# Optimization experiments

Hardware: AMD Instinct MI355X
Metric: run time of the kernel (lower is better)

The kernel has to match this reference:

```python
import jax, jax.numpy as jnp
import numpy as np

B, S, H, U = 32, 2048, 1024, 1024


def setup_inputs() -> dict:
    key = jax.random.key(0)
    ks = jax.random.split(key, 5)
    sc = 1.0 / np.sqrt(H)
    return {
        "hidden_t": jax.random.normal(ks[0], (B, H), jnp.float32),
        "hiddens": jax.random.normal(ks[1], (B, S, H), jnp.float32),
        "W1": jax.random.normal(ks[2], (H, U), jnp.float32) * sc,
        "b1": jnp.zeros((U,), jnp.float32),
        "W2": jax.random.normal(ks[3], (H, U), jnp.float32) * sc,
        "b2": jnp.zeros((U,), jnp.float32),
        "V": jax.random.normal(ks[4], (U, 1), jnp.float32) * sc,
        "bV": jnp.zeros((1,), jnp.float32),
    }


def reference(hidden_t, hiddens, W1, b1, W2, b2, V, bV):
    # proj of encoder states: [B,S,U]; proj of decoder state broadcast over time: [B,1,U]
    keys = jnp.einsum("bsh,hu->bsu", hiddens, W1) + b1
    query = (hidden_t @ W2 + b2)[:, None, :]
    score = jnp.tanh(keys + query) @ V + bV            # [B,S,1]
    attention_weights = jax.nn.softmax(score, axis=1)  # softmax over seq axis
    context_vector = jnp.sum(attention_weights * hiddens, axis=1)  # [B,H]
    return context_vector, attention_weights
```

## Files before the change

kernel.cpp:

```cpp
#include <hip/hip_runtime.h>
#include <hip/hip_bf16.h>
#include <cstdint>

#define S_LEN 2048
#define B_SZ  32
#define H_DIM 1024
#define U_DIM 1024

#define BM 128
#define BN 128
#define BK 64

using short8  = __attribute__((ext_vector_type(8))) short;
using floatx4 = __attribute__((ext_vector_type(4))) float;

typedef __attribute__((address_space(3))) void lds_void;
typedef const __attribute__((address_space(1))) void glb_void;
#define GLD16(g, s) __builtin_amdgcn_global_load_lds((glb_void*)(g), (lds_void*)(s), 16, 0, 0)

__device__ __forceinline__ unsigned short f32_to_bf16_rne(float f) {
    unsigned int u = __float_as_uint(f);
    unsigned int r = (u + 0x7fffu + ((u >> 16) & 1u)) >> 16;
    return (unsigned short)r;
}

__global__ __launch_bounds__(256)
void cast_hiddens_kernel(const float* __restrict__ src, unsigned short* __restrict__ dst) {
    const size_t i = ((size_t)blockIdx.x * 256 + threadIdx.x) * 8;
    float4 a = *(const float4*)(src + i);
    float4 b = *(const float4*)(src + i + 4);
    ushort4 lo, hi;
    lo.x = f32_to_bf16_rne(a.x); lo.y = f32_to_bf16_rne(a.y);
    lo.z = f32_to_bf16_rne(a.z); lo.w = f32_to_bf16_rne(a.w);
    hi.x = f32_to_bf16_rne(b.x); hi.y = f32_to_bf16_rne(b.y);
    hi.z = f32_to_bf16_rne(b.z); hi.w = f32_to_bf16_rne(b.w);
    *(ushort4*)(dst + i)     = lo;
    *(ushort4*)(dst + i + 4) = hi;
}

__global__ void transpose_cast_w1(const float* __restrict__ W1,
                                  unsigned short* __restrict__ W1t) {
    __shared__ float tile[32][33];
    const int tx = threadIdx.x, ty = threadIdx.y;
    const int u0 = blockIdx.x * 32, h0 = blockIdx.y * 32;
#pragma unroll
    for (int i = 0; i < 4; ++i)
        tile[ty * 4 + i][tx] = W1[(size_t)(h0 + ty * 4 + i) * U_DIM + u0 + tx];
    __syncthreads();
#pragma unroll
    for (int i = 0; i < 4; ++i)
        W1t[(size_t)(u0 + ty * 4 + i) * H_DIM + h0 + tx] =
            f32_to_bf16_rne(tile[tx][ty * 4 + i]);
}

__global__ __launch_bounds__(128)
void query_kernel_v2(const float* __restrict__ hidden_t,
                     const float* __restrict__ W2,
                     const float* __restrict__ b1,
                     const float* __restrict__ b2,
                     float* __restrict__ query) {
    const int b  = blockIdx.z;
    const int hc = blockIdx.y;
    const int u  = blockIdx.x * 128 + threadIdx.x;
    const float* ht = hidden_t + b * H_DIM + hc * 128;
    const float* w  = W2 + (size_t)hc * 128 * U_DIM + u;
    float acc = (hc == 0) ? (b1[u] + b2[u]) : 0.f;
#pragma unroll 8
    for (int h = 0; h < 128; ++h)
        acc = fmaf(ht[h], w[(size_t)h * U_DIM], acc);
    atomicAdd(&query[b * U_DIM + u], acc);
}

__device__ __forceinline__ void score_epilogue(const floatx4 acc[4][4],
                                               const float* __restrict__ qrow,
                                               const float* __restrict__ V,
                                               float* __restrict__ scores,
                                               int m0, int n0, int wr, int wc, int q, int r) {
#pragma unroll
    for (int mt = 0; mt < 4; ++mt) {
#pragma unroll
        for (int reg = 0; reg < 4; ++reg) {
            float sum = 0.f;
#pragma unroll
            for (int nt = 0; nt < 4; ++nt) {
                const int c = n0 + wc * 64 + nt * 16 + r;
                float x = acc[mt][nt][reg] + qrow[c];
                x = fminf(fmaxf(x, -15.f), 15.f);
                float e = __expf(2.f * x);
                float t = (e - 1.f) / (e + 1.f);
                sum = fmaf(t, V[c], sum);
            }
            sum += __shfl_xor(sum, 1);
            sum += __shfl_xor(sum, 2);
            sum += __shfl_xor(sum, 4);
            sum += __shfl_xor(sum, 8);
            if (r == 0)
                atomicAdd(&scores[m0 + wr * 64 + mt * 16 + q * 4 + reg], sum);
        }
    }
}

__global__ __launch_bounds__(256)
void keys_score_v4(const unsigned short* __restrict__ hb,
                   const unsigned short* __restrict__ W1t,
                   const float* __restrict__ query,
                   const float* __restrict__ V,
                   float* __restrict__ scores) {
    __shared__ unsigned short As[BM * BK];
    __shared__ unsigned short Bs[BN * BK];

    const int tid = threadIdx.x;
    const int w = tid >> 6, l = tid & 63;
    const int q = l >> 4, r = l & 15;
    const int wr = w >> 1, wc = w & 1;

    const int bid = blockIdx.x;
    const int col      = (bid >> 3) & 7;
    const int row_band = ((bid >> 6) << 3) | (bid & 7);
    const int m0 = row_band * BM;
    const int n0 = col * BN;

    const int srow   = l >> 3;
    const int gchunk = ((l & 7) ^ srow) * 8;

    const unsigned short* gA = hb  + ((size_t)(m0 + w * 8 + srow) << 10) + gchunk;
    const unsigned short* gB = W1t + ((size_t)(n0 + w * 8 + srow) << 10) + gchunk;
    unsigned short* lA = &As[(w * 8) * BK];
    unsigned short* lB = &Bs[(w * 8) * BK];

    floatx4 acc[4][4];
#pragma unroll
    for (int mt = 0; mt < 4; ++mt)
#pragma unroll
        for (int nt = 0; nt < 4; ++nt)
            acc[mt][nt] = (floatx4){0.f, 0.f, 0.f, 0.f};

    const int r7 = r & 7;
    for (int kt = 0; kt < H_DIM / BK; ++kt) {
#pragma unroll
        for (int i = 0; i < 4; ++i) {
            GLD16(gA + ((size_t)(i * 32) << 10), lA + i * 32 * BK);
            GLD16(gB + ((size_t)(i * 32) << 10), lB + i * 32 * BK);
        }
        gA += BK; gB += BK;

        __syncthreads();

#pragma unroll
        for (int kh = 0; kh < 2; ++kh) {
            short8 af[4], bfr[4];
#pragma unroll
            for (int mt = 0; mt < 4; ++mt)
                af[mt] = *(const short8*)
                    &As[(wr * 64 + mt * 16 + r) * BK + (((kh << 2) | q) ^ r7) * 8];
#pragma unroll
            for (int nt = 0; nt < 4; ++nt)
                bfr[nt] = *(const short8*)
                    &Bs[(wc * 64 + nt * 16 + r) * BK + (((kh << 2) | q) ^ r7) * 8];
#pragma unroll
            for (int mt = 0; mt < 4; ++mt)
#pragma unroll
                for (int nt = 0; nt < 4; ++nt)
                    acc[mt][nt] = __builtin_amdgcn_mfma_f32_16x16x32_bf16(
                        af[mt], bfr[nt], acc[mt][nt], 0, 0, 0);
        }

        __syncthreads();
    }

    const float* qrow = query + (m0 >> 11) * U_DIM;
    score_epilogue(acc, qrow, V, scores, m0, n0, wr, wc, q, r);
}

__global__ __launch_bounds__(256)
void keys_score_v1(const float* __restrict__ hiddens,
                   const unsigned short* __restrict__ W1t,
                   const float* __restrict__ query,
                   const float* __restrict__ V,
                   float* __restrict__ scores) {
    __shared__ unsigned short As[BM][40];
    __shared__ unsigned short Bs[BN][40];
    const int tid = threadIdx.x;
    const int lane = tid & 63, wave = tid >> 6;
    const int q = lane >> 4, r = lane & 15;
    const int wr = wave >> 1, wc = wave & 1;
    const int m0 = blockIdx.y * BM, n0 = blockIdx.x * BN;
    const int arow = tid >> 3, achunk = tid & 7;
    const int brow = tid >> 2, bchunk = tid & 3;
    floatx4 acc[4][4];
#pragma unroll
    for (int mt = 0; mt < 4; ++mt)
#pragma unroll
        for (int nt = 0; nt < 4; ++nt)
            acc[mt][nt] = (floatx4){0.f, 0.f, 0.f, 0.f};
    for (int kt = 0; kt < H_DIM / 32; ++kt) {
        const float* ag = hiddens + (size_t)(m0 + arow) * H_DIM + kt * 32 + achunk * 4;
#pragma unroll
        for (int i = 0; i < 4; ++i) {
            float4 f = *(const float4*)(ag + (size_t)i * 32 * H_DIM);
            ushort4 h;
            h.x = f32_to_bf16_rne(f.x); h.y = f32_to_bf16_rne(f.y);
            h.z = f32_to_bf16_rne(f.z); h.w = f32_to_bf16_rne(f.w);
            *(ushort4*)&As[arow + i * 32][achunk * 4] = h;
        }
        const unsigned short* bg = W1t + (size_t)(n0 + brow) * H_DIM + kt * 32 + bchunk * 8;
#pragma unroll
        for (int i = 0; i < 2; ++i)
            *(uint4*)&Bs[brow + i * 64][bchunk * 8] = *(const uint4*)(bg + (size_t)i * 64 * H_DIM);
        __syncthreads();
        short8 af[4], bfr[4];
#pragma unroll
        for (int mt = 0; mt < 4; ++mt)
            af[mt] = *(const short8*)&As[wr * 64 + mt * 16 + r][q * 8];
#pragma unroll
        for (int nt = 0; nt < 4; ++nt)
            bfr[nt] = *(const short8*)&Bs[wc * 64 + nt * 16 + r][q * 8];
#pragma unroll
        for (int mt = 0; mt < 4; ++mt)
#pragma unroll
            for (int nt = 0; nt < 4; ++nt)
                acc[mt][nt] = __builtin_amdgcn_mfma_f32_16x16x32_bf16(
                    af[mt], bfr[nt], acc[mt][nt], 0, 0, 0);
        __syncthreads();
    }
    const float* qrow = query + (m0 >> 11) * U_DIM;
    score_epilogue(acc, qrow, V, scores, m0, n0, wr, wc, q, r);
}

__global__ void softmax_kernel(const float* __restrict__ scores,
                               float* __restrict__ wout) {
    const int b = blockIdx.x, tid = threadIdx.x;
    const int wave = tid >> 6, lane = tid & 63;
    const float* src = scores + b * S_LEN;
    float v[8];
    float m = -1e30f;
#pragma unroll
    for (int i = 0; i < 8; ++i) { v[i] = src[tid + i * 256]; m = fmaxf(m, v[i]); }
#pragma unroll
    for (int off = 32; off >= 1; off >>= 1) m = fmaxf(m, __shfl_xor(m, off));
    __shared__ float red[4];
    if (lane == 0) red[wave] = m;
    __syncthreads();
    m = fmaxf(fmaxf(red[0], red[1]), fmaxf(red[2], red[3]));
    __syncthreads();
    float s = 0.f;
#pragma unroll
    for (int i = 0; i < 8; ++i) { v[i] = __expf(v[i] - m); s += v[i]; }
#pragma unroll
    for (int off = 32; off >= 1; off >>= 1) s += __shfl_xor(s, off);
    if (lane == 0) red[wave] = s;
    __syncthreads();
    s = red[0] + red[1] + red[2] + red[3];
    const float inv = 1.f / s;
#pragma unroll
    for (int i = 0; i < 8; ++i) wout[b * S_LEN + tid + i * 256] = v[i] * inv;
}

__global__ __launch_bounds__(256)
void context_kernel(const float* __restrict__ weights,
                    const float* __restrict__ hiddens,
                    float* __restrict__ out_ctx) {
    const int b = blockIdx.y;
    const int sc = blockIdx.x;
    const int h4 = threadIdx.x * 4;
    const float* wrow = weights + b * S_LEN + sc * 32;
    const float* hbase = hiddens + ((size_t)b * S_LEN + sc * 32) * H_DIM + h4;
    float4 acc = make_float4(0.f, 0.f, 0.f, 0.f);
#pragma unroll 4
    for (int s = 0; s < 32; ++s) {
        const float w = wrow[s];
        float4 hv = *(const float4*)(hbase + (size_t)s * H_DIM);
        acc.x = fmaf(w, hv.x, acc.x);
        acc.y = fmaf(w, hv.y, acc.y);
        acc.z = fmaf(w, hv.z, acc.z);
        acc.w = fmaf(w, hv.w, acc.w);
    }
    float* o = out_ctx + b * H_DIM + h4;
    atomicAdd(o + 0, acc.x);
    atomicAdd(o + 1, acc.y);
    atomicAdd(o + 2, acc.z);
    atomicAdd(o + 3, acc.w);
}

extern "C" void kernel_launch(void* const* d_in, const int* in_sizes, int n_in,
                              void* d_out, int out_size, void* d_ws, size_t ws_size,
                              hipStream_t stream) {
    const float* hidden_t = (const float*)d_in[0];
    const float* hiddens  = (const float*)d_in[1];
    const float* W1       = (const float*)d_in[2];
    const float* b1       = (const float*)d_in[3];
    const float* W2       = (const float*)d_in[4];
    const float* b2       = (const float*)d_in[5];
    const float* V        = (const float*)d_in[6];

    float* out_ctx = (float*)d_out;
    float* out_w   = (float*)d_out + B_SZ * H_DIM;

    char* ws = (char*)d_ws;
    unsigned short* W1t = (unsigned short*)ws;
    float* query  = (float*)(ws + (2u << 20));
    float* scores = query + B_SZ * U_DIM;
    unsigned short* hb = (unsigned short*)(ws + (4u << 20));
    const size_t need = (4u << 20) + (size_t)B_SZ * S_LEN * H_DIM * 2;

    hipMemsetAsync(query,  0, (size_t)B_SZ * U_DIM * sizeof(float), stream);
    hipMemsetAsync(scores, 0, (size_t)B_SZ * S_LEN * sizeof(float), stream);
    hipMemsetAsync(out_ctx, 0, (size_t)B_SZ * H_DIM * sizeof(float), stream);

    transpose_cast_w1<<<dim3(32, 32), dim3(32, 8), 0, stream>>>(W1, W1t);
    query_kernel_v2<<<dim3(8, 8, B_SZ), 128, 0, stream>>>(hidden_t, W2, b1, b2, query);

    if (ws_size >= need) {
        cast_hiddens_kernel<<<32768, 256, 0, stream>>>(hiddens, hb);
        keys_score_v4<<<(U_DIM / BN) * ((B_SZ * S_LEN) / BM), 256, 0, stream>>>(
            hb, W1t, query, V, scores);
    } else {
        keys_score_v1<<<dim3(U_DIM / 128, (B_SZ * S_LEN) / BM), 256, 0, stream>>>(
            hiddens, W1t, query, V, scores);
    }

    softmax_kernel<<<B_SZ, 256, 0, stream>>>(scores, out_w);
    context_kernel<<<dim3(S_LEN / 32, B_SZ), 256, 0, stream>>>(out_w, hiddens, out_ctx);
}
```

Before: 660.7 us.

## Fuse softmax normalization into context pass and replace atomics with partial reduction

Softmax now only computes per-batch max and inverse sum. The context kernel recomputes normalized weights, writes them out, and accumulates 128-row chunks into per-chunk partial buffers instead of atomically adding. A small reduce kernel sums the partials, which removes the global atomics and the output memset. The trade-off is fewer, longer-running blocks in the context pass and an extra launch.

Measured after the change: 648.1 us. No clear change (-1.9%).

```diff
diff --git a/kernel.cpp b/kernel.cpp
--- a/kernel.cpp
+++ b/kernel.cpp
@@ -227,8 +227,9 @@
     score_epilogue(acc, qrow, V, scores, m0, n0, wr, wc, q, r);
 }
 
-__global__ void softmax_kernel(const float* __restrict__ scores,
-                               float* __restrict__ wout) {
+__global__ __launch_bounds__(256)
+void softmax_stats_kernel(const float* __restrict__ scores,
+                          float2* __restrict__ stats) {
     const int b = blockIdx.x, tid = threadIdx.x;
     const int wave = tid >> 6, lane = tid & 63;
     const float* src = scores + b * S_LEN;
@@ -245,41 +246,61 @@
     __syncthreads();
     float s = 0.f;
 #pragma unroll
-    for (int i = 0; i < 8; ++i) { v[i] = __expf(v[i] - m); s += v[i]; }
+    for (int i = 0; i < 8; ++i) s += __expf(v[i] - m);
 #pragma unroll
     for (int off = 32; off >= 1; off >>= 1) s += __shfl_xor(s, off);
     if (lane == 0) red[wave] = s;
     __syncthreads();
-    s = red[0] + red[1] + red[2] + red[3];
-    const float inv = 1.f / s;
-#pragma unroll
-    for (int i = 0; i < 8; ++i) wout[b * S_LEN + tid + i * 256] = v[i] * inv;
-}
-
-__global__ __launch_bounds__(256)
-void context_kernel(const float* __restrict__ weights,
-                    const float* __restrict__ hiddens,
-                    float* __restrict__ out_ctx) {
-    const int b = blockIdx.y;
-    const int sc = blockIdx.x;
-    const int h4 = threadIdx.x * 4;
-    const float* wrow = weights + b * S_LEN + sc * 32;
-    const float* hbase = hiddens + ((size_t)b * S_LEN + sc * 32) * H_DIM + h4;
+    if (tid == 0) {
+        s = red[0] + red[1] + red[2] + red[3];
+        stats[b] = make_float2(m, 1.f / s);
+    }
+}
+
+__global__ __launch_bounds__(256)
+void context_partial_kernel(const float* __restrict__ scores,
+                            const float2* __restrict__ stats,
+                            const float* __restrict__ hiddens,
+                            float* __restrict__ out_w,
+                            float* __restrict__ partial) {
+    const int b = blockIdx.y, sc = blockIdx.x;
+    const int tid = threadIdx.x;
+    __shared__ float wsm[128];
+
+    const float2 st = stats[b];
+    if (tid < 128) {
+        const int s = sc * 128 + tid;
+        const float w = __expf(scores[b * S_LEN + s] - st.x) * st.y;
+        wsm[tid] = w;
+        out_w[b * S_LEN + s] = w;
+    }
+    __syncthreads();
+
+    const float* hbase = hiddens + ((size_t)b * S_LEN + sc * 128) * H_DIM + tid * 4;
     float4 acc = make_float4(0.f, 0.f, 0.f, 0.f);
 #pragma unroll 4
-    for (int s = 0; s < 32; ++s) {
-        const float w = wrow[s];
+    for (int s = 0; s < 128; ++s) {
+        const float w = wsm[s];
         float4 hv = *(const float4*)(hbase + (size_t)s * H_DIM);
         acc.x = fmaf(w, hv.x, acc.x);
         acc.y = fmaf(w, hv.y, acc.y);
         acc.z = fmaf(w, hv.z, acc.z);
         acc.w = fmaf(w, hv.w, acc.w);
     }
-    float* o = out_ctx + b * H_DIM + h4;
-    atomicAdd(o + 0, acc.x);
-    atomicAdd(o + 1, acc.y);
-    atomicAdd(o + 2, acc.z);
-    atomicAdd(o + 3, acc.w);
+    *(float4*)(partial + ((size_t)(b * 16 + sc) << 10) + tid * 4) = acc;
+}
+
+__global__ __launch_bounds__(256)
+void context_reduce_kernel(const float* __restrict__ partial,
+                           float* __restrict__ out_ctx) {
+    const int b = blockIdx.x, tid = threadIdx.x;
+    float4 acc = make_float4(0.f, 0.f, 0.f, 0.f);
+#pragma unroll
+    for (int sc = 0; sc < 16; ++sc) {
+        float4 p = *(const float4*)(partial + ((size_t)(b * 16 + sc) << 10) + tid * 4);
+        acc.x += p.x; acc.y += p.y; acc.z += p.z; acc.w += p.w;
+    }
+    *(float4*)(out_ctx + b * H_DIM + tid * 4) = acc;
 }
 
 extern "C" void kernel_launch(void* const* d_in, const int* in_sizes, int n_in,
@@ -298,14 +319,15 @@
 
     char* ws = (char*)d_ws;
     unsigned short* W1t = (unsigned short*)ws;
-    float* query  = (float*)(ws + (2u << 20));
-    float* scores = query + B_SZ * U_DIM;
-    unsigned short* hb = (unsigned short*)(ws + (4u << 20));
-    const size_t need = (4u << 20) + (size_t)B_SZ * S_LEN * H_DIM * 2;
+    float*  query   = (float*)(ws + (2u << 20));
+    float*  scores  = query + B_SZ * U_DIM;
+    float2* stats   = (float2*)(scores + B_SZ * S_LEN);
+    float*  partial = (float*)(ws + (3u << 20));
+    unsigned short* hb = (unsigned short*)(ws + (6u << 20));
+    const size_t need = (6u << 20) + (size_t)B_SZ * S_LEN * H_DIM * 2;
 
     hipMemsetAsync(query,  0, (size_t)B_SZ * U_DIM * sizeof(float), stream);
     hipMemsetAsync(scores, 0, (size_t)B_SZ * S_LEN * sizeof(float), stream);
-    hipMemsetAsync(out_ctx, 0, (size_t)B_SZ * H_DIM * sizeof(float), stream);
 
     transpose_cast_w1<<<dim3(32, 32), dim3(32, 8), 0, stream>>>(W1, W1t);
     query_kernel_v2<<<dim3(8, 8, B_SZ), 128, 0, stream>>>(hidden_t, W2, b1, b2, query);
@@ -319,6 +341,8 @@
             hiddens, W1t, query, V, scores);
     }
 
-    softmax_kernel<<<B_SZ, 256, 0, stream>>>(scores, out_w);
-    context_kernel<<<dim3(S_LEN / 32, B_SZ), 256, 0, stream>>>(out_w, hiddens, out_ctx);
-}
+    softmax_stats_kernel<<<B_SZ, 256, 0, stream>>>(scores, stats);
+    context_partial_kernel<<<dim3(16, B_SZ), 256, 0, stream>>>(
+        scores, stats, hiddens, out_w, partial);
+    context_reduce_kernel<<<B_SZ, 256, 0, stream>>>(partial, out_ctx);
+}
```
